# Performance work log

Measured on AMD Instinct MI355X. Metric: run time of the kernel, lower is better.

The kernel has to match this reference:

```python
import jax, jax.numpy as jnp
import numpy as np

N = 8192
FEAT = 128
HID = 128
EMB = 128
NHEADS = 2
RO_HID = 256
G_EMB = 128
ALPHA = 0.2          # LeakyReLU negative slope
NEG_INF = -9e15      # matches -9000000000000000.0 in the torch source


def _xavier(k, shape, gain=1.0):
    fan_in, fan_out = shape[-2], shape[-1]
    s = gain * np.sqrt(2.0 / (fan_in + fan_out))
    return jax.random.normal(k, shape, jnp.float32) * jnp.float32(s)


def setup_inputs() -> dict:
    key = jax.random.key(0)
    ks = jax.random.split(key, 10)
    adj = jax.random.randint(ks[0], (N, N), 0, 2, jnp.int32)          # dense 0/1 adjacency
    x = jax.random.normal(ks[1], (N, FEAT), jnp.float32)
    W_heads = _xavier(ks[2], (NHEADS, FEAT, HID), gain=1.414)
    a_heads = _xavier(ks[3], (NHEADS, 2 * HID, 1), gain=1.414)
    W_out = _xavier(ks[4], (NHEADS * HID, EMB), gain=1.414)
    a_out = _xavier(ks[5], (2 * EMB, 1), gain=1.414)
    ge_w1 = _xavier(ks[6], (FEAT + EMB, RO_HID))
    ge_b1 = jnp.zeros((RO_HID,), jnp.float32)
    ge_w2 = _xavier(ks[7], (RO_HID, G_EMB))
    ge_b2 = jnp.zeros((G_EMB,), jnp.float32)
    return dict(adj=adj, feature_matrix=x, W_heads=W_heads, a_heads=a_heads,
                W_out=W_out, a_out=a_out, ge_w1=ge_w1, ge_b1=ge_b1,
                ge_w2=ge_w2, ge_b2=ge_b2, supply=0)


def _gat_layer(x, mask, W, a, concat):
    # Faithful to GraphAttentionLayer: e_ij = leakyrelu([Wh_i || Wh_j] @ a).
    # The concat-then-matmul decomposes exactly as Wh@a[:F] + (Wh@a[F:])^T,
    # avoiding the O(N^2 * 2F) a_input tensor while computing identical math.
    Wh = x @ W                                   # [N, F]
    F_out = W.shape[1]
    f1 = (Wh @ a[:F_out]).squeeze(-1)            # [N]
    f2 = (Wh @ a[F_out:]).squeeze(-1)            # [N]
    e = jax.nn.leaky_relu(f1[:, None] + f2[None, :], ALPHA)   # [N, N]
    e = jnp.where(mask, e, jnp.float32(NEG_INF))
    att = jax.nn.softmax(e, axis=1)              # dropout is identity in eval mode
    h = att @ Wh                                 # [N, F]
    return jax.nn.elu(h) if concat else h


def reference(adj, feature_matrix, W_heads, a_heads, W_out, a_out,
              ge_w1, ge_b1, ge_w2, ge_b2, supply):
    mask = adj > 0
    # GAT: multi-head layer 1 (concat), then out_att (no concat) + elu
    heads = [_gat_layer(feature_matrix, mask, W_heads[i], a_heads[i], True)
             for i in range(NHEADS)]
    h = jnp.concatenate(heads, axis=1)           # [N, NHEADS*HID]
    node_emb = jax.nn.elu(_gat_layer(h, mask, W_out, a_out, False))  # [N, EMB]
    # GraphEmb readout (mode='mean')
    combined = jnp.concatenate([feature_matrix, node_emb], axis=1)   # [N, FEAT+EMB]
    h1 = jax.nn.relu(combined @ ge_w1 + ge_b1)
    h2 = jax.nn.relu(h1 @ ge_w2 + ge_b2)
    graph_emb = jnp.mean(h2, axis=0)             # [G_EMB]
    return node_emb, graph_emb
```

## Files before the change

### kernel.cpp

```cpp
#include <hip/hip_runtime.h>
#include <hip/hip_bf16.h>

typedef unsigned short u16;
typedef __attribute__((ext_vector_type(4))) float f32x4;
typedef __attribute__((ext_vector_type(8))) short bf16x8;
typedef __attribute__((ext_vector_type(4))) unsigned short u16x4;

#define N 8192
#define LOG2E 1.4426950408889634f

__device__ __forceinline__ float bf2f(u16 u){
  union { float f; unsigned int i; } v; v.i = ((unsigned int)u) << 16; return v.f;
}
__device__ __forceinline__ u16 f2bf(float f){
  union { float f; unsigned int i; } v; v.f = f;
  unsigned int r = v.i + 0x7fffu + ((v.i >> 16) & 1u);
  return (u16)(r >> 16);
}
__device__ __forceinline__ f32x4 mfma16(bf16x8 a, bf16x8 b, f32x4 c){
  return __builtin_amdgcn_mfma_f32_16x16x32_bf16(a, b, c, 0, 0, 0);
}

__global__ __launch_bounds__(256) void k_pack(const int* __restrict__ adj,
                                              unsigned long long* __restrict__ packed){
  const int wid = blockIdx.x * 4 + (threadIdx.x >> 6);
  const int lane = threadIdx.x & 63;
  const size_t base = (size_t)wid * 128;
  #pragma unroll 4
  for (int g = 0; g < 128; ++g){
    const size_t grp = base + g;
    const int v = adj[grp * 64 + lane];
    const unsigned long long m = __ballot(v != 0);
    if (lane == 0){
      const unsigned int lo = (unsigned int)m, hi = (unsigned int)(m >> 32);
      const unsigned int olo = __builtin_amdgcn_perm(hi, lo, 0x05010400u);
      const unsigned int ohi = __builtin_amdgcn_perm(hi, lo, 0x07030602u);
      packed[grp] = ((unsigned long long)ohi << 32) | olo;
    }
  }
}

__global__ __launch_bounds__(256) void k_x2bf(const float* __restrict__ x,
                                              u16* __restrict__ xbf, u16* __restrict__ comb){
  const int idx = blockIdx.x * 256 + threadIdx.x;
  f32x4 v = ((const f32x4*)x)[idx];
  u16x4 h;
  #pragma unroll
  for (int e = 0; e < 4; ++e) h[e] = f2bf(v[e]);
  ((u16x4*)xbf)[idx] = h;
  const int i = idx >> 5, c4 = (idx & 31) * 4;
  *(u16x4*)(comb + (size_t)i * 256 + c4) = h;
}

__global__ void k_transpose(const float* __restrict__ src, u16* __restrict__ dst,
                            int K, int Ncols){
  const size_t boff = (size_t)blockIdx.y * K * Ncols;
  const int idx = blockIdx.x * 256 + threadIdx.x;
  if (idx >= K * Ncols) return;
  const int n = idx / K, k = idx % K;
  dst[boff + idx] = f2bf(src[boff + (size_t)k * Ncols + n]);
}

__global__ __launch_bounds__(256) void k_wa(const float* __restrict__ Wh, const float* __restrict__ ah,
                                            const float* __restrict__ Wo, const float* __restrict__ ao,
                                            float* __restrict__ wa){
  const int z = blockIdx.x, t = threadIdx.x;
  if (z < 2){
    if (t < 128){
      float a1 = 0.f, a2 = 0.f;
      for (int c = 0; c < 128; ++c){
        const float w = Wh[(size_t)z * 16384 + t * 128 + c];
        a1 += w * ah[z * 256 + c];
        a2 += w * ah[z * 256 + 128 + c];
      }
      wa[z * 128 + t] = a1; wa[256 + z * 128 + t] = a2;
    }
  } else {
    if (t < 256){
      float a1 = 0.f, a2 = 0.f;
      for (int c = 0; c < 128; ++c){
        const float w = Wo[(size_t)t * 128 + c];
        a1 += w * ao[c];
        a2 += w * ao[128 + c];
      }
      wa[512 + t] = a1; wa[768 + t] = a2;
    }
  }
}

__global__ __launch_bounds__(256) void k_gemv1(const float* __restrict__ x, const float* __restrict__ wa,
                                               float* __restrict__ f1s, float* __restrict__ f2s){
  const int h = blockIdx.y;
  const float* wa1 = wa + h * 128;
  const float* wa2 = wa + 256 + h * 128;
  const int lane = threadIdx.x & 63, w = threadIdx.x >> 6;
  const int r16 = lane & 15, g4 = lane >> 4;
  const int row = blockIdx.x * 16 + w * 4 + g4;
  const float* xr = x + (size_t)row * 128 + r16 * 8;
  f32x4 x0 = *(const f32x4*)(xr);
  f32x4 x1 = *(const f32x4*)(xr + 4);
  f32x4 wA0 = *(const f32x4*)(wa1 + r16 * 8);
  f32x4 wA1 = *(const f32x4*)(wa1 + r16 * 8 + 4);
  f32x4 wB0 = *(const f32x4*)(wa2 + r16 * 8);
  f32x4 wB1 = *(const f32x4*)(wa2 + r16 * 8 + 4);
  float d1 = 0.f, d2 = 0.f;
  #pragma unroll
  for (int e = 0; e < 4; ++e){
    d1 += x0[e] * wA0[e] + x1[e] * wA1[e];
    d2 += x0[e] * wB0[e] + x1[e] * wB1[e];
  }
  d1 += __shfl_xor(d1, 1); d1 += __shfl_xor(d1, 2); d1 += __shfl_xor(d1, 4); d1 += __shfl_xor(d1, 8);
  d2 += __shfl_xor(d2, 1); d2 += __shfl_xor(d2, 2); d2 += __shfl_xor(d2, 4); d2 += __shfl_xor(d2, 8);
  if (r16 == 0){
    f1s[(size_t)h * N + row] = d1 * LOG2E;
    f2s[(size_t)h * N + row] = d2 * LOG2E;
  }
}

__global__ __launch_bounds__(256) void k_gemv2(const u16* __restrict__ hbf,
                                               const float* __restrict__ wao1, const float* __restrict__ wao2,
                                               float* __restrict__ f1s, float* __restrict__ f2s){
  const int lane = threadIdx.x & 63, w = threadIdx.x >> 6;
  const int r16 = lane & 15, g4 = lane >> 4;
  const int row = blockIdx.x * 16 + w * 4 + g4;
  bf16x8 h0 = *(const bf16x8*)(hbf + (size_t)row * 256 + r16 * 16);
  bf16x8 h1 = *(const bf16x8*)(hbf + (size_t)row * 256 + r16 * 16 + 8);
  float d1 = 0.f, d2 = 0.f;
  #pragma unroll
  for (int e = 0; e < 8; ++e){
    const float v0 = bf2f((u16)h0[e]), v1 = bf2f((u16)h1[e]);
    d1 += v0 * wao1[r16 * 16 + e] + v1 * wao1[r16 * 16 + 8 + e];
    d2 += v0 * wao2[r16 * 16 + e] + v1 * wao2[r16 * 16 + 8 + e];
  }
  d1 += __shfl_xor(d1, 1); d1 += __shfl_xor(d1, 2); d1 += __shfl_xor(d1, 4); d1 += __shfl_xor(d1, 8);
  d2 += __shfl_xor(d2, 1); d2 += __shfl_xor(d2, 2); d2 += __shfl_xor(d2, 4); d2 += __shfl_xor(d2, 8);
  if (r16 == 0){
    f1s[row] = d1 * LOG2E;
    f2s[row] = d2 * LOG2E;
  }
}

__global__ __launch_bounds__(256) void k_fmax(const float* __restrict__ f2s, float* __restrict__ fmax){
  const int h = blockIdx.x;
  const float* f = f2s + (size_t)h * N;
  float m = -3e38f;
  for (int i = threadIdx.x; i < N; i += 256) m = fmaxf(m, f[i]);
  m = fmaxf(m, __shfl_xor(m, 1));  m = fmaxf(m, __shfl_xor(m, 2));
  m = fmaxf(m, __shfl_xor(m, 4));  m = fmaxf(m, __shfl_xor(m, 8));
  m = fmaxf(m, __shfl_xor(m, 16)); m = fmaxf(m, __shfl_xor(m, 32));
  __shared__ float sm[4];
  if ((threadIdx.x & 63) == 0) sm[threadIdx.x >> 6] = m;
  __syncthreads();
  if (threadIdx.x == 0) fmax[h] = fmaxf(fmaxf(sm[0], sm[1]), fmaxf(sm[2], sm[3]));
}

__global__ __launch_bounds__(256) void k_gemm_at(const u16* __restrict__ A_all, const u16* __restrict__ B,
                                                 u16* __restrict__ outT_all, int K){
  const int head = blockIdx.y;
  const u16* A = A_all + (size_t)head * 128 * K;
  u16* outT = outT_all + (size_t)head * 128 * N;
  const int lane = threadIdx.x & 63, w = threadIdx.x >> 6;
  const int r16 = lane & 15, g4 = lane >> 4;
  const size_t ib = (size_t)blockIdx.x * 64 + w * 16;
  f32x4 acc[8];
  #pragma unroll
  for (int cg = 0; cg < 8; ++cg) acc[cg] = (f32x4){0,0,0,0};
  for (int kk = 0; kk < K; kk += 32){
    bf16x8 b = *(const bf16x8*)(B + (ib + r16) * (size_t)K + kk + g4 * 8);
    #pragma unroll
    for (int cg = 0; cg < 8; ++cg){
      bf16x8 a = *(const bf16x8*)(A + (size_t)(cg * 16 + r16) * K + kk + g4 * 8);
      acc[cg] = mfma16(a, b, acc[cg]);
    }
  }
  #pragma unroll
  for (int cg = 0; cg < 8; ++cg)
    #pragma unroll
    for (int q = 0; q < 4; ++q)
      outT[(size_t)(cg * 16 + g4 * 4 + q) * N + ib + r16] = f2bf(acc[cg][q]);
}

template<int S>
__global__ __launch_bounds__(64, 3) void k_attn(
    const unsigned char* __restrict__ pk,
    const u16* __restrict__ whT_all,
    const float* __restrict__ f1_all, const float* __restrict__ f2_all,
    const float* __restrict__ fmax_all,
    u16* __restrict__ part, float* __restrict__ pl)
{
  const int h = blockIdx.z;
  const int s = blockIdx.y;
  const u16* whT = whT_all + (size_t)h * 128 * N;
  const float* f2 = f2_all + (size_t)h * N;
  const float fmax = fmax_all[h];
  const int lane = threadIdx.x;
  const int r16 = lane & 15, g4 = lane >> 4;
  const size_t ibase = (size_t)blockIdx.x * 32;
  const int t0 = (s * 128) / S, t1 = ((s + 1) * 128) / S;

  float c1[2], c2[2];
  f32x4 acc[2][8];
  f32x4 accl[2];
  #pragma unroll
  for (int rg = 0; rg < 2; ++rg){
    const float f1v = f1_all[(size_t)h * N + ibase + rg * 16 + r16];
    const float y = f1v + fmax;
    const float mrow = fmaxf(y, 0.2f * y);
    c1[rg] = f1v - mrow;
    c2[rg] = fmaf(0.2f, f1v, -mrow);
    accl[rg] = (f32x4){0,0,0,0};
    #pragma unroll
    for (int ct = 0; ct < 8; ++ct) acc[rg][ct] = (f32x4){0,0,0,0};
  }
  bf16x8 ones;
  #pragma unroll
  for (int e = 0; e < 8; ++e) ones[e] = (short)0x3F80;

  const unsigned char* pkr0 = pk + (ibase + r16) * 1024 + g4 * 2;
  const unsigned char* pkr1 = pkr0 + 16 * 1024;
  const float* f2p = f2 + g4 * 8;
  unsigned int bc0 = *(const unsigned short*)(pkr0 + t0 * 8);
  unsigned int bc1 = *(const unsigned short*)(pkr1 + t0 * 8);
  f32x4 f2r0 = *(const f32x4*)(f2p + t0 * 64);
  f32x4 f2r1 = *(const f32x4*)(f2p + t0 * 64 + 4);
  f32x4 f2r2 = *(const f32x4*)(f2p + t0 * 64 + 32);
  f32x4 f2r3 = *(const f32x4*)(f2p + t0 * 64 + 36);

  for (int t = t0; t < t1; ++t){
    const u16* bp = whT + (size_t)r16 * N + t * 64 + g4 * 8;
    bf16x8 b0[8];
    #pragma unroll
    for (int ct = 0; ct < 8; ++ct) b0[ct] = *(const bf16x8*)(bp + (size_t)ct * 16 * N);
    unsigned int bn0, bn1; f32x4 f2n0, f2n1, f2n2, f2n3;
    if (t + 1 < t1){
      bn0 = *(const unsigned short*)(pkr0 + (t + 1) * 8);
      bn1 = *(const unsigned short*)(pkr1 + (t + 1) * 8);
      f2n0 = *(const f32x4*)(f2p + (t + 1) * 64);
      f2n1 = *(const f32x4*)(f2p + (t + 1) * 64 + 4);
      f2n2 = *(const f32x4*)(f2p + (t + 1) * 64 + 32);
      f2n3 = *(const f32x4*)(f2p + (t + 1) * 64 + 36);
    } else {
      bn0 = bc0; bn1 = bc1; f2n0 = f2r0; f2n1 = f2r1; f2n2 = f2r2; f2n3 = f2r3;
    }
    bf16x8 pa[2][2];
    #pragma unroll
    for (int k2 = 0; k2 < 2; ++k2){
      const f32x4 fa = k2 ? f2r2 : f2r0;
      const f32x4 fb = k2 ? f2r3 : f2r1;
      const float fsv[8] = {fa[0], fa[1], fa[2], fa[3], fb[0], fb[1], fb[2], fb[3]};
      #pragma unroll
      for (int rg = 0; rg < 2; ++rg){
        const unsigned int bb = ((rg ? bc1 : bc0) >> (k2 * 8)) & 0xFFu;
        union { __hip_bfloat162 h2[4]; bf16x8 v8; } u;
        #pragma unroll
        for (int xp = 0; xp < 4; ++xp){
          const float s0 = fsv[2 * xp], s1 = fsv[2 * xp + 1];
          float p0 = __builtin_amdgcn_exp2f(fmaxf(s0 + c1[rg], fmaf(s0, 0.2f, c2[rg])));
          float p1 = __builtin_amdgcn_exp2f(fmaxf(s1 + c1[rg], fmaf(s1, 0.2f, c2[rg])));
          p0 = ((bb >> (2 * xp)) & 1u) ? p0 : 0.f;
          p1 = ((bb >> (2 * xp + 1)) & 1u) ? p1 : 0.f;
          u.h2[xp] = __float22bfloat162_rn(make_float2(p0, p1));
        }
        pa[rg][k2] = u.v8;
        accl[rg] = mfma16(pa[rg][k2], ones, accl[rg]);
      }
    }
    #pragma unroll
    for (int ct = 0; ct < 8; ++ct){
      acc[0][ct] = mfma16(pa[0][0], b0[ct], acc[0][ct]);
      acc[1][ct] = mfma16(pa[1][0], b0[ct], acc[1][ct]);
    }
    #pragma unroll
    for (int ct = 0; ct < 8; ++ct){
      bf16x8 b1 = *(const bf16x8*)(bp + (size_t)ct * 16 * N + 32);
      acc[0][ct] = mfma16(pa[0][1], b1, acc[0][ct]);
      acc[1][ct] = mfma16(pa[1][1], b1, acc[1][ct]);
    }
    bc0 = bn0; bc1 = bn1; f2r0 = f2n0; f2r1 = f2n1; f2r2 = f2n2; f2r3 = f2n3;
  }

  const int plane = h * S + s;
  u16* pp = part + (size_t)plane * (size_t)N * 128;
  #pragma unroll
  for (int rg = 0; rg < 2; ++rg){
    if (r16 == 0){
      #pragma unroll
      for (int q = 0; q < 4; ++q)
        pl[(size_t)plane * N + ibase + rg * 16 + g4 * 4 + q] = accl[rg][q];
    }
    #pragma unroll
    for (int ct = 0; ct < 8; ++ct)
      #pragma unroll
      for (int q = 0; q < 4; ++q)
        pp[(ibase + rg * 16 + g4 * 4 + q) * 128 + ct * 16 + r16] = f2bf(acc[rg][ct][q]);
  }
}

template<int S, bool L2>
__global__ __launch_bounds__(256) void k_attn_merge(
    const u16* __restrict__ part, const float* __restrict__ pl,
    u16* __restrict__ hbf, float* __restrict__ nodeout, u16* __restrict__ comb)
{
  const int h = blockIdx.y;
  const int idx = blockIdx.x * 256 + threadIdx.x;
  const int i = idx >> 5, c4 = (idx & 31) * 4;
  f32x4 a = (f32x4){0,0,0,0};
  float L = 0.f;
  #pragma unroll
  for (int s = 0; s < S; ++s){
    const size_t plane = h * S + s;
    u16x4 v = *(const u16x4*)(part + plane * (size_t)N * 128 + (size_t)i * 128 + c4);
    a[0] += bf2f(v[0]); a[1] += bf2f(v[1]); a[2] += bf2f(v[2]); a[3] += bf2f(v[3]);
    L += pl[plane * (size_t)N + i];
  }
  const float linv = 1.f / L;
  u16x4 hv;
  #pragma unroll
  for (int e = 0; e < 4; ++e){
    float o = a[e] * linv;
    o = (o > 0.f) ? o : (__expf(o) - 1.f);
    a[e] = o;
    hv[e] = f2bf(o);
  }
  if constexpr (!L2){
    *(u16x4*)(hbf + (size_t)i * 256 + h * 128 + c4) = hv;
  } else {
    *(f32x4*)(nodeout + (size_t)i * 128 + c4) = a;
    *(u16x4*)(comb + (size_t)i * 256 + 128 + c4) = hv;
  }
}

template<bool STORE, bool COLSUM>
__global__ __launch_bounds__(256) void k_gemm_row(
    const u16* __restrict__ A, const u16* __restrict__ BT,
    const float* __restrict__ bias,
    u16* __restrict__ out, float* __restrict__ csum,
    int K, int Ntot)
{
  const int lane = threadIdx.x & 63, w = threadIdx.x >> 6;
  const int r16 = lane & 15, g4 = lane >> 4;
  const size_t rbase = (size_t)blockIdx.x * 64 + w * 16;
  const int cbase = blockIdx.y * 128;
  f32x4 acc[8];
  #pragma unroll
  for (int ct = 0; ct < 8; ++ct) acc[ct] = (f32x4){0,0,0,0};
  for (int kk = 0; kk < K; kk += 32){
    bf16x8 af = *(const bf16x8*)(A + (rbase + r16) * (size_t)K + kk + g4 * 8);
    #pragma unroll
    for (int ct = 0; ct < 8; ++ct){
      bf16x8 bfr = *(const bf16x8*)(BT + (size_t)(cbase + ct * 16 + r16) * K + kk + g4 * 8);
      acc[ct] = mfma16(af, bfr, acc[ct]);
    }
  }
  #pragma unroll
  for (int ct = 0; ct < 8; ++ct){
    const float bv = bias[cbase + ct * 16 + r16];
    float sacc = 0.f;
    #pragma unroll
    for (int q = 0; q < 4; ++q){
      float v = acc[ct][q] + bv;
      v = fmaxf(v, 0.f);
      if constexpr (STORE)
        out[(rbase + g4 * 4 + q) * (size_t)Ntot + cbase + ct * 16 + r16] = f2bf(v);
      sacc += v;
    }
    if constexpr (COLSUM){
      sacc += __shfl_xor(sacc, 16); sacc += __shfl_xor(sacc, 32);
      if (lane < 16) atomicAdd(&csum[cbase + ct * 16 + lane], sacc);
    }
  }
}

__global__ void k_final(const float* __restrict__ csum, float* __restrict__ out){
  out[threadIdx.x] = csum[threadIdx.x] * (1.f / 8192.f);
}

extern "C" void kernel_launch(void* const* d_in, const int* in_sizes, int n_in,
                              void* d_out, int out_size, void* d_ws, size_t ws_size,
                              hipStream_t stream) {
  const int*   adj = (const int*)d_in[0];
  const float* x   = (const float*)d_in[1];
  const float* Wh  = (const float*)d_in[2];
  const float* ah  = (const float*)d_in[3];
  const float* Wo  = (const float*)d_in[4];
  const float* ao  = (const float*)d_in[5];
  const float* g1  = (const float*)d_in[6];
  const float* b1  = (const float*)d_in[7];
  const float* g2  = (const float*)d_in[8];
  const float* b2  = (const float*)d_in[9];
  float* outp = (float*)d_out;
  char* ws = (char*)d_ws;

  constexpr size_t PK   = 0;
  constexpr size_t PART = 8388608;
  constexpr size_t PL   = 33554432;
  constexpr size_t XBF  = 33947648;
  constexpr size_t WHT1 = 36044800;
  constexpr size_t WHT2 = 40239104;
  constexpr size_t HBF  = 42336256;
  constexpr size_t COMB = 46530560;
  constexpr size_t H1RO = 50724864;
  constexpr size_t F1S  = 54919168;
  constexpr size_t F2S  = 54984704;
  constexpr size_t FMAX = 55050240;
  constexpr size_t CSUM = 55050496;
  constexpr size_t WTH  = 55051008;
  constexpr size_t WOT  = 55116544;
  constexpr size_t G1T  = 55182080;
  constexpr size_t G2T  = 55313152;
  constexpr size_t WA   = 55378688;

  hipMemsetAsync(ws + CSUM, 0, 512, stream);

  k_pack<<<2048, 256, 0, stream>>>(adj, (unsigned long long*)(ws + PK));
  k_x2bf<<<1024, 256, 0, stream>>>(x, (u16*)(ws + XBF), (u16*)(ws + COMB));
  k_transpose<<<dim3(64, 2), 256, 0, stream>>>(Wh, (u16*)(ws + WTH), 128, 128);
  k_transpose<<<dim3(128, 1), 256, 0, stream>>>(Wo, (u16*)(ws + WOT), 256, 128);
  k_transpose<<<dim3(256, 1), 256, 0, stream>>>(g1, (u16*)(ws + G1T), 256, 256);
  k_transpose<<<dim3(128, 1), 256, 0, stream>>>(g2, (u16*)(ws + G2T), 256, 128);
  k_wa<<<3, 256, 0, stream>>>(Wh, ah, Wo, ao, (float*)(ws + WA));

  k_gemv1<<<dim3(512, 2), 256, 0, stream>>>(x, (const float*)(ws + WA),
                                            (float*)(ws + F1S), (float*)(ws + F2S));
  k_fmax<<<2, 256, 0, stream>>>((const float*)(ws + F2S), (float*)(ws + FMAX));
  k_gemm_at<<<dim3(128, 2), 256, 0, stream>>>((const u16*)(ws + WTH), (const u16*)(ws + XBF),
                                              (u16*)(ws + WHT1), 128);
  k_attn<6><<<dim3(256, 6, 2), 64, 0, stream>>>(
      (const unsigned char*)(ws + PK), (const u16*)(ws + WHT1),
      (const float*)(ws + F1S), (const float*)(ws + F2S), (const float*)(ws + FMAX),
      (u16*)(ws + PART), (float*)(ws + PL));
  k_attn_merge<6, false><<<dim3(1024, 2), 256, 0, stream>>>(
      (const u16*)(ws + PART), (const float*)(ws + PL),
      (u16*)(ws + HBF), nullptr, nullptr);

  k_gemv2<<<dim3(512, 1), 256, 0, stream>>>((const u16*)(ws + HBF),
      (const float*)(ws + WA) + 512, (const float*)(ws + WA) + 768,
      (float*)(ws + F1S), (float*)(ws + F2S));
  k_fmax<<<1, 256, 0, stream>>>((const float*)(ws + F2S), (float*)(ws + FMAX));
  k_gemm_at<<<dim3(128, 1), 256, 0, stream>>>((const u16*)(ws + WOT), (const u16*)(ws + HBF),
                                              (u16*)(ws + WHT2), 256);
  k_attn<12><<<dim3(256, 12, 1), 64, 0, stream>>>(
      (const unsigned char*)(ws + PK), (const u16*)(ws + WHT2),
      (const float*)(ws + F1S), (const float*)(ws + F2S), (const float*)(ws + FMAX),
      (u16*)(ws + PART), (float*)(ws + PL));
  k_attn_merge<12, true><<<dim3(1024, 1), 256, 0, stream>>>(
      (const u16*)(ws + PART), (const float*)(ws + PL),
      nullptr, outp, (u16*)(ws + COMB));

  k_gemm_row<true, false><<<dim3(128, 2), 256, 0, stream>>>(
      (const u16*)(ws + COMB), (const u16*)(ws + G1T), b1,
      (u16*)(ws + H1RO), nullptr, 256, 256);
  k_gemm_row<false, true><<<dim3(128, 1), 256, 0, stream>>>(
      (const u16*)(ws + H1RO), (const u16*)(ws + G2T), b2,
      nullptr, (float*)(ws + CSUM), 256, 128);
  k_final<<<1, 128, 0, stream>>>((const float*)(ws + CSUM), outp + (size_t)N * 128);
}
```

Baseline: 790.1 us.

## Fuse prep kernels, fold column max into GEMV atomics, reshape attention tiling

Merges the bf16 conversion, weight transposes, wa precompute and zero-initialisation into a single prep kernel, removing several launches and the memset. The separate column-max kernels are dropped: each GEMV wave now does an atomicMax on an order-preserving uint key. The attention kernel moves from 64-thread blocks handling 32 rows each to 256-thread blocks where each wave handles 16 rows, so each wave uses fewer registers but the per-wave reuse of the loaded Wh tiles is halved. Partial outputs are written in an MFMA-fragment tile layout that the merge kernel reads back with matching index arithmetic, giving coalesced stores.

```diff
diff --git a/kernel.cpp b/kernel.cpp
--- a/kernel.cpp
+++ b/kernel.cpp
@@ -19,6 +19,14 @@
 }
 __device__ __forceinline__ f32x4 mfma16(bf16x8 a, bf16x8 b, f32x4 c){
   return __builtin_amdgcn_mfma_f32_16x16x32_bf16(a, b, c, 0, 0, 0);
+}
+__device__ __forceinline__ unsigned int fkey_enc(float f){
+  unsigned int u = __float_as_uint(f);
+  return (u & 0x80000000u) ? ~u : (u | 0x80000000u);
+}
+__device__ __forceinline__ float fkey_dec(unsigned int k){
+  unsigned int u = (k & 0x80000000u) ? (k ^ 0x80000000u) : ~k;
+  return __uint_as_float(u);
 }
 
 __global__ __launch_bounds__(256) void k_pack(const int* __restrict__ adj,
@@ -40,56 +48,74 @@
   }
 }
 
-__global__ __launch_bounds__(256) void k_x2bf(const float* __restrict__ x,
-                                              u16* __restrict__ xbf, u16* __restrict__ comb){
-  const int idx = blockIdx.x * 256 + threadIdx.x;
-  f32x4 v = ((const f32x4*)x)[idx];
-  u16x4 h;
-  #pragma unroll
-  for (int e = 0; e < 4; ++e) h[e] = f2bf(v[e]);
-  ((u16x4*)xbf)[idx] = h;
-  const int i = idx >> 5, c4 = (idx & 31) * 4;
-  *(u16x4*)(comb + (size_t)i * 256 + c4) = h;
-}
-
-__global__ void k_transpose(const float* __restrict__ src, u16* __restrict__ dst,
-                            int K, int Ncols){
-  const size_t boff = (size_t)blockIdx.y * K * Ncols;
-  const int idx = blockIdx.x * 256 + threadIdx.x;
-  if (idx >= K * Ncols) return;
-  const int n = idx / K, k = idx % K;
-  dst[boff + idx] = f2bf(src[boff + (size_t)k * Ncols + n]);
-}
-
-__global__ __launch_bounds__(256) void k_wa(const float* __restrict__ Wh, const float* __restrict__ ah,
-                                            const float* __restrict__ Wo, const float* __restrict__ ao,
-                                            float* __restrict__ wa){
-  const int z = blockIdx.x, t = threadIdx.x;
-  if (z < 2){
-    if (t < 128){
-      float a1 = 0.f, a2 = 0.f;
-      for (int c = 0; c < 128; ++c){
-        const float w = Wh[(size_t)z * 16384 + t * 128 + c];
-        a1 += w * ah[z * 256 + c];
-        a2 += w * ah[z * 256 + 128 + c];
+__global__ __launch_bounds__(256) void k_prep(
+    const float* __restrict__ x, const float* __restrict__ Wh, const float* __restrict__ Wo,
+    const float* __restrict__ g1, const float* __restrict__ g2,
+    const float* __restrict__ ah, const float* __restrict__ ao,
+    u16* __restrict__ xbf, u16* __restrict__ comb,
+    u16* __restrict__ wth, u16* __restrict__ wot,
+    u16* __restrict__ g1t, u16* __restrict__ g2t,
+    float* __restrict__ wa, unsigned int* __restrict__ fkey, float* __restrict__ csum)
+{
+  const int b = blockIdx.x, t = threadIdx.x;
+  if (b < 1024){
+    const int idx = b * 256 + t;
+    f32x4 v = ((const f32x4*)x)[idx];
+    u16x4 h;
+    #pragma unroll
+    for (int e = 0; e < 4; ++e) h[e] = f2bf(v[e]);
+    ((u16x4*)xbf)[idx] = h;
+    const int i = idx >> 5, c4 = (idx & 31) * 4;
+    *(u16x4*)(comb + (size_t)i * 256 + c4) = h;
+  } else if (b < 1152){
+    const int rel = (b - 1024) * 256 + t;
+    const int head = rel >> 14, win = rel & 16383;
+    const int n = win >> 7, k = win & 127;
+    wth[rel] = f2bf(Wh[(head << 14) + k * 128 + n]);
+  } else if (b < 1280){
+    const int rel = (b - 1152) * 256 + t;
+    const int n = rel >> 8, k = rel & 255;
+    wot[rel] = f2bf(Wo[k * 128 + n]);
+  } else if (b < 1536){
+    const int rel = (b - 1280) * 256 + t;
+    const int n = rel >> 8, k = rel & 255;
+    g1t[rel] = f2bf(g1[k * 256 + n]);
+  } else if (b < 1664){
+    const int rel = (b - 1536) * 256 + t;
+    const int n = rel >> 8, k = rel & 255;
+    g2t[rel] = f2bf(g2[k * 128 + n]);
+  } else if (b < 1667){
+    const int z = b - 1664;
+    if (z < 2){
+      if (t < 128){
+        float a1 = 0.f, a2 = 0.f;
+        for (int c = 0; c < 128; ++c){
+          const float w = Wh[(size_t)z * 16384 + t * 128 + c];
+          a1 += w * ah[z * 256 + c];
+          a2 += w * ah[z * 256 + 128 + c];
+        }
+        wa[z * 128 + t] = a1; wa[256 + z * 128 + t] = a2;
       }
-      wa[z * 128 + t] = a1; wa[256 + z * 128 + t] = a2;
+    } else {
+      if (t < 256){
+        float a1 = 0.f, a2 = 0.f;
+        for (int c = 0; c < 128; ++c){
+          const float w = Wo[(size_t)t * 128 + c];
+          a1 += w * ao[c];
+          a2 += w * ao[128 + c];
+        }
+        wa[512 + t] = a1; wa[768 + t] = a2;
+      }
     }
   } else {
-    if (t < 256){
-      float a1 = 0.f, a2 = 0.f;
-      for (int c = 0; c < 128; ++c){
-        const float w = Wo[(size_t)t * 128 + c];
-        a1 += w * ao[c];
-        a2 += w * ao[128 + c];
-      }
-      wa[512 + t] = a1; wa[768 + t] = a2;
-    }
+    if (t < 128) csum[t] = 0.f;
+    if (t < 4) fkey[t] = 0u;
   }
 }
 
 __global__ __launch_bounds__(256) void k_gemv1(const float* __restrict__ x, const float* __restrict__ wa,
-                                               float* __restrict__ f1s, float* __restrict__ f2s){
+                                               float* __restrict__ f1s, float* __restrict__ f2s,
+                                               unsigned int* __restrict__ fkey){
   const int h = blockIdx.y;
   const float* wa1 = wa + h * 128;
   const float* wa2 = wa + 256 + h * 128;
@@ -111,15 +137,20 @@
   }
   d1 += __shfl_xor(d1, 1); d1 += __shfl_xor(d1, 2); d1 += __shfl_xor(d1, 4); d1 += __shfl_xor(d1, 8);
   d2 += __shfl_xor(d2, 1); d2 += __shfl_xor(d2, 2); d2 += __shfl_xor(d2, 4); d2 += __shfl_xor(d2, 8);
+  const float d1s = d1 * LOG2E, d2s = d2 * LOG2E;
   if (r16 == 0){
-    f1s[(size_t)h * N + row] = d1 * LOG2E;
-    f2s[(size_t)h * N + row] = d2 * LOG2E;
-  }
+    f1s[(size_t)h * N + row] = d1s;
+    f2s[(size_t)h * N + row] = d2s;
+  }
+  float m = d2s;
+  m = fmaxf(m, __shfl_xor(m, 16)); m = fmaxf(m, __shfl_xor(m, 32));
+  if (lane == 0) atomicMax(fkey + h, fkey_enc(m));
 }
 
 __global__ __launch_bounds__(256) void k_gemv2(const u16* __restrict__ hbf,
                                                const float* __restrict__ wao1, const float* __restrict__ wao2,
-                                               float* __restrict__ f1s, float* __restrict__ f2s){
+                                               float* __restrict__ f1s, float* __restrict__ f2s,
+                                               unsigned int* __restrict__ fkey){
   const int lane = threadIdx.x & 63, w = threadIdx.x >> 6;
   const int r16 = lane & 15, g4 = lane >> 4;
   const int row = blockIdx.x * 16 + w * 4 + g4;
@@ -134,24 +165,14 @@
   }
   d1 += __shfl_xor(d1, 1); d1 += __shfl_xor(d1, 2); d1 += __shfl_xor(d1, 4); d1 += __shfl_xor(d1, 8);
   d2 += __shfl_xor(d2, 1); d2 += __shfl_xor(d2, 2); d2 += __shfl_xor(d2, 4); d2 += __shfl_xor(d2, 8);
+  const float d1s = d1 * LOG2E, d2s = d2 * LOG2E;
   if (r16 == 0){
-    f1s[row] = d1 * LOG2E;
-    f2s[row] = d2 * LOG2E;
-  }
-}
-
-__global__ __launch_bounds__(256) void k_fmax(const float* __restrict__ f2s, float* __restrict__ fmax){
-  const int h = blockIdx.x;
-  const float* f = f2s + (size_t)h * N;
-  float m = -3e38f;
-  for (int i = threadIdx.x; i < N; i += 256) m = fmaxf(m, f[i]);
-  m = fmaxf(m, __shfl_xor(m, 1));  m = fmaxf(m, __shfl_xor(m, 2));
-  m = fmaxf(m, __shfl_xor(m, 4));  m = fmaxf(m, __shfl_xor(m, 8));
+    f1s[row] = d1s;
+    f2s[row] = d2s;
+  }
+  float m = d2s;
   m = fmaxf(m, __shfl_xor(m, 16)); m = fmaxf(m, __shfl_xor(m, 32));
-  __shared__ float sm[4];
-  if ((threadIdx.x & 63) == 0) sm[threadIdx.x >> 6] = m;
-  __syncthreads();
-  if (threadIdx.x == 0) fmax[h] = fmaxf(fmaxf(sm[0], sm[1]), fmaxf(sm[2], sm[3]));
+  if (lane == 0) atomicMax(fkey, fkey_enc(m));
 }
 
 __global__ __launch_bounds__(256) void k_gemm_at(const u16* __restrict__ A_all, const u16* __restrict__ B,
@@ -181,46 +202,41 @@
 }
 
 template<int S>
-__global__ __launch_bounds__(64, 3) void k_attn(
+__global__ __launch_bounds__(256, 4) void k_attn(
     const unsigned char* __restrict__ pk,
     const u16* __restrict__ whT_all,
     const float* __restrict__ f1_all, const float* __restrict__ f2_all,
-    const float* __restrict__ fmax_all,
+    const unsigned int* __restrict__ fkey,
     u16* __restrict__ part, float* __restrict__ pl)
 {
   const int h = blockIdx.z;
   const int s = blockIdx.y;
   const u16* whT = whT_all + (size_t)h * 128 * N;
   const float* f2 = f2_all + (size_t)h * N;
-  const float fmax = fmax_all[h];
-  const int lane = threadIdx.x;
+  const float fmax = fkey_dec(fkey[h]);
+  const int w = threadIdx.x >> 6;
+  const int lane = threadIdx.x & 63;
   const int r16 = lane & 15, g4 = lane >> 4;
-  const size_t ibase = (size_t)blockIdx.x * 32;
+  const int tile_row = blockIdx.x * 4 + w;
+  const size_t ibase = (size_t)tile_row * 16;
   const int t0 = (s * 128) / S, t1 = ((s + 1) * 128) / S;
 
-  float c1[2], c2[2];
-  f32x4 acc[2][8];
-  f32x4 accl[2];
-  #pragma unroll
-  for (int rg = 0; rg < 2; ++rg){
-    const float f1v = f1_all[(size_t)h * N + ibase + rg * 16 + r16];
-    const float y = f1v + fmax;
-    const float mrow = fmaxf(y, 0.2f * y);
-    c1[rg] = f1v - mrow;
-    c2[rg] = fmaf(0.2f, f1v, -mrow);
-    accl[rg] = (f32x4){0,0,0,0};
-    #pragma unroll
-    for (int ct = 0; ct < 8; ++ct) acc[rg][ct] = (f32x4){0,0,0,0};
-  }
+  const float f1v = f1_all[(size_t)h * N + ibase + r16];
+  const float y = f1v + fmax;
+  const float mrow = fmaxf(y, 0.2f * y);
+  const float c1 = f1v - mrow;
+  const float c2 = fmaf(0.2f, f1v, -mrow);
+  f32x4 acc[8];
+  f32x4 accl = (f32x4){0,0,0,0};
+  #pragma unroll
+  for (int ct = 0; ct < 8; ++ct) acc[ct] = (f32x4){0,0,0,0};
   bf16x8 ones;
   #pragma unroll
   for (int e = 0; e < 8; ++e) ones[e] = (short)0x3F80;
 
-  const unsigned char* pkr0 = pk + (ibase + r16) * 1024 + g4 * 2;
-  const unsigned char* pkr1 = pkr0 + 16 * 1024;
+  const unsigned char* pkr = pk + (ibase + r16) * 1024 + g4 * 2;
   const float* f2p = f2 + g4 * 8;
-  unsigned int bc0 = *(const unsigned short*)(pkr0 + t0 * 8);
-  unsigned int bc1 = *(const unsigned short*)(pkr1 + t0 * 8);
+  unsigned int bc = *(const unsigned short*)(pkr + t0 * 8);
   f32x4 f2r0 = *(const f32x4*)(f2p + t0 * 64);
   f32x4 f2r1 = *(const f32x4*)(f2p + t0 * 64 + 4);
   f32x4 f2r2 = *(const f32x4*)(f2p + t0 * 64 + 32);
@@ -231,68 +247,58 @@
     bf16x8 b0[8];
     #pragma unroll
     for (int ct = 0; ct < 8; ++ct) b0[ct] = *(const bf16x8*)(bp + (size_t)ct * 16 * N);
-    unsigned int bn0, bn1; f32x4 f2n0, f2n1, f2n2, f2n3;
+    unsigned int bn; f32x4 f2n0, f2n1, f2n2, f2n3;
     if (t + 1 < t1){
-      bn0 = *(const unsigned short*)(pkr0 + (t + 1) * 8);
-      bn1 = *(const unsigned short*)(pkr1 + (t + 1) * 8);
+      bn = *(const unsigned short*)(pkr + (t + 1) * 8);
       f2n0 = *(const f32x4*)(f2p + (t + 1) * 64);
       f2n1 = *(const f32x4*)(f2p + (t + 1) * 64 + 4);
       f2n2 = *(const f32x4*)(f2p + (t + 1) * 64 + 32);
       f2n3 = *(const f32x4*)(f2p + (t + 1) * 64 + 36);
     } else {
-      bn0 = bc0; bn1 = bc1; f2n0 = f2r0; f2n1 = f2r1; f2n2 = f2r2; f2n3 = f2r3;
-    }
-    bf16x8 pa[2][2];
+      bn = bc; f2n0 = f2r0; f2n1 = f2r1; f2n2 = f2r2; f2n3 = f2r3;
+    }
+    bf16x8 pa[2];
     #pragma unroll
     for (int k2 = 0; k2 < 2; ++k2){
       const f32x4 fa = k2 ? f2r2 : f2r0;
       const f32x4 fb = k2 ? f2r3 : f2r1;
       const float fsv[8] = {fa[0], fa[1], fa[2], fa[3], fb[0], fb[1], fb[2], fb[3]};
+      const unsigned int bb = (bc >> (k2 * 8)) & 0xFFu;
+      union { __hip_bfloat162 h2[4]; bf16x8 v8; } u;
       #pragma unroll
-      for (int rg = 0; rg < 2; ++rg){
-        const unsigned int bb = ((rg ? bc1 : bc0) >> (k2 * 8)) & 0xFFu;
-        union { __hip_bfloat162 h2[4]; bf16x8 v8; } u;
-        #pragma unroll
-        for (int xp = 0; xp < 4; ++xp){
-          const float s0 = fsv[2 * xp], s1 = fsv[2 * xp + 1];
-          float p0 = __builtin_amdgcn_exp2f(fmaxf(s0 + c1[rg], fmaf(s0, 0.2f, c2[rg])));
-          float p1 = __builtin_amdgcn_exp2f(fmaxf(s1 + c1[rg], fmaf(s1, 0.2f, c2[rg])));
-          p0 = ((bb >> (2 * xp)) & 1u) ? p0 : 0.f;
-          p1 = ((bb >> (2 * xp + 1)) & 1u) ? p1 : 0.f;
-          u.h2[xp] = __float22bfloat162_rn(make_float2(p0, p1));
-        }
-        pa[rg][k2] = u.v8;
-        accl[rg] = mfma16(pa[rg][k2], ones, accl[rg]);
+      for (int xp = 0; xp < 4; ++xp){
+        const float s0 = fsv[2 * xp], s1 = fsv[2 * xp + 1];
+        float p0 = __builtin_amdgcn_exp2f(fmaxf(s0 + c1, fmaf(s0, 0.2f, c2)));
+        float p1 = __builtin_amdgcn_exp2f(fmaxf(s1 + c1, fmaf(s1, 0.2f, c2)));
+        p0 = ((bb >> (2 * xp)) & 1u) ? p0 : 0.f;
+        p1 = ((bb >> (2 * xp + 1)) & 1u) ? p1 : 0.f;
+        u.h2[xp] = __float22bfloat162_rn(make_float2(p0, p1));
       }
-    }
-    #pragma unroll
-    for (int ct = 0; ct < 8; ++ct){
-      acc[0][ct] = mfma16(pa[0][0], b0[ct], acc[0][ct]);
-      acc[1][ct] = mfma16(pa[1][0], b0[ct], acc[1][ct]);
-    }
+      pa[k2] = u.v8;
+      accl = mfma16(pa[k2], ones, accl);
+    }
+    #pragma unroll
+    for (int ct = 0; ct < 8; ++ct)
+      acc[ct] = mfma16(pa[0], b0[ct], acc[ct]);
     #pragma unroll
     for (int ct = 0; ct < 8; ++ct){
       bf16x8 b1 = *(const bf16x8*)(bp + (size_t)ct * 16 * N + 32);
-      acc[0][ct] = mfma16(pa[0][1], b1, acc[0][ct]);
-      acc[1][ct] = mfma16(pa[1][1], b1, acc[1][ct]);
-    }
-    bc0 = bn0; bc1 = bn1; f2r0 = f2n0; f2r1 = f2n1; f2r2 = f2n2; f2r3 = f2n3;
+      acc[ct] = mfma16(pa[1], b1, acc[ct]);
+    }
+    bc = bn; f2r0 = f2n0; f2r1 = f2n1; f2r2 = f2n2; f2r3 = f2n3;
   }
 
   const int plane = h * S + s;
-  u16* pp = part + (size_t)plane * (size_t)N * 128;
-  #pragma unroll
-  for (int rg = 0; rg < 2; ++rg){
-    if (r16 == 0){
-      #pragma unroll
-      for (int q = 0; q < 4; ++q)
-        pl[(size_t)plane * N + ibase + rg * 16 + g4 * 4 + q] = accl[rg][q];
-    }
-    #pragma unroll
-    for (int ct = 0; ct < 8; ++ct)
-      #pragma unroll
-      for (int q = 0; q < 4; ++q)
-        pp[(ibase + rg * 16 + g4 * 4 + q) * 128 + ct * 16 + r16] = f2bf(acc[rg][ct][q]);
+  u16* pp = part + ((size_t)plane * 512 + tile_row) * 2048;
+  #pragma unroll
+  for (int ct = 0; ct < 8; ++ct)
+    #pragma unroll
+    for (int q = 0; q < 4; ++q)
+      pp[(ct * 4 + q) * 64 + lane] = f2bf(acc[ct][q]);
+  if (r16 == 0){
+    #pragma unroll
+    for (int q = 0; q < 4; ++q)
+      pl[(size_t)plane * N + ibase + g4 * 4 + q] = accl[q];
   }
 }
 
@@ -304,12 +310,14 @@
   const int h = blockIdx.y;
   const int idx = blockIdx.x * 256 + threadIdx.x;
   const int i = idx >> 5, c4 = (idx & 31) * 4;
+  const int tile = i >> 4, r = i & 15;
+  const size_t off = (size_t)tile * 2048 + (size_t)(((c4 >> 4) * 4 + (r & 3)) * 64 + ((r >> 2) & 3) * 16 + (c4 & 15));
   f32x4 a = (f32x4){0,0,0,0};
   float L = 0.f;
   #pragma unroll
   for (int s = 0; s < S; ++s){
     const size_t plane = h * S + s;
-    u16x4 v = *(const u16x4*)(part + plane * (size_t)N * 128 + (size_t)i * 128 + c4);
+    u16x4 v = *(const u16x4*)(part + plane * (size_t)(N * 128) + off);
     a[0] += bf2f(v[0]); a[1] += bf2f(v[1]); a[2] += bf2f(v[2]); a[3] += bf2f(v[3]);
     L += pl[plane * (size_t)N + i];
   }
@@ -402,32 +410,27 @@
   constexpr size_t H1RO = 50724864;
   constexpr size_t F1S  = 54919168;
   constexpr size_t F2S  = 54984704;
-  constexpr size_t FMAX = 55050240;
-  constexpr size_t CSUM = 55050496;
+  constexpr size_t CSUM = 55050240;
   constexpr size_t WTH  = 55051008;
   constexpr size_t WOT  = 55116544;
   constexpr size_t G1T  = 55182080;
   constexpr size_t G2T  = 55313152;
   constexpr size_t WA   = 55378688;
-
-  hipMemsetAsync(ws + CSUM, 0, 512, stream);
+  constexpr size_t FKEY = 55382784;
 
   k_pack<<<2048, 256, 0, stream>>>(adj, (unsigned long long*)(ws + PK));
-  k_x2bf<<<1024, 256, 0, stream>>>(x, (u16*)(ws + XBF), (u16*)(ws + COMB));
-  k_transpose<<<dim3(64, 2), 256, 0, stream>>>(Wh, (u16*)(ws + WTH), 128, 128);
-  k_transpose<<<dim3(128, 1), 256, 0, stream>>>(Wo, (u16*)(ws + WOT), 256, 128);
-  k_transpose<<<dim3(256, 1), 256, 0, stream>>>(g1, (u16*)(ws + G1T), 256, 256);
-  k_transpose<<<dim3(128, 1), 256, 0, stream>>>(g2, (u16*)(ws + G2T), 256, 128);
-  k_wa<<<3, 256, 0, stream>>>(Wh, ah, Wo, ao, (float*)(ws + WA));
+  k_prep<<<1668, 256, 0, stream>>>(x, Wh, Wo, g1, g2, ah, ao,
+      (u16*)(ws + XBF), (u16*)(ws + COMB), (u16*)(ws + WTH), (u16*)(ws + WOT),
+      (u16*)(ws + G1T), (u16*)(ws + G2T),
+      (float*)(ws + WA), (unsigned int*)(ws + FKEY), (float*)(ws + CSUM));
 
   k_gemv1<<<dim3(512, 2), 256, 0, stream>>>(x, (const float*)(ws + WA),
-                                            (float*)(ws + F1S), (float*)(ws + F2S));
-  k_fmax<<<2, 256, 0, stream>>>((const float*)(ws + F2S), (float*)(ws + FMAX));
+      (float*)(ws + F1S), (float*)(ws + F2S), (unsigned int*)(ws + FKEY));
   k_gemm_at<<<dim3(128, 2), 256, 0, stream>>>((const u16*)(ws + WTH), (const u16*)(ws + XBF),
                                               (u16*)(ws + WHT1), 128);
-  k_attn<6><<<dim3(256, 6, 2), 64, 0, stream>>>(
+  k_attn<6><<<dim3(128, 6, 2), 256, 0, stream>>>(
       (const unsigned char*)(ws + PK), (const u16*)(ws + WHT1),
-      (const float*)(ws + F1S), (const float*)(ws + F2S), (const float*)(ws + FMAX),
+      (const float*)(ws + F1S), (const float*)(ws + F2S), (const unsigned int*)(ws + FKEY),
       (u16*)(ws + PART), (float*)(ws + PL));
   k_attn_merge<6, false><<<dim3(1024, 2), 256, 0, stream>>>(
       (const u16*)(ws + PART), (const float*)(ws + PL),
@@ -435,13 +438,12 @@
 
   k_gemv2<<<dim3(512, 1), 256, 0, stream>>>((const u16*)(ws + HBF),
       (const float*)(ws + WA) + 512, (const float*)(ws + WA) + 768,
-      (float*)(ws + F1S), (float*)(ws + F2S));
-  k_fmax<<<1, 256, 0, stream>>>((const float*)(ws + F2S), (float*)(ws + FMAX));
+      (float*)(ws + F1S), (float*)(ws + F2S), (unsigned int*)(ws + FKEY) + 2);
   k_gemm_at<<<dim3(128, 1), 256, 0, stream>>>((const u16*)(ws + WOT), (const u16*)(ws + HBF),
                                               (u16*)(ws + WHT2), 256);
-  k_attn<12><<<dim3(256, 12, 1), 64, 0, stream>>>(
+  k_attn<12><<<dim3(128, 12, 1), 256, 0, stream>>>(
       (const unsigned char*)(ws + PK), (const u16*)(ws + WHT2),
-      (const float*)(ws + F1S), (const float*)(ws + F2S), (const float*)(ws + FMAX),
+      (const float*)(ws + F1S), (const float*)(ws + F2S), (const unsigned int*)(ws + FKEY) + 2,
       (u16*)(ws + PART), (float*)(ws + PL));
   k_attn_merge<12, true><<<dim3(1024, 1), 256, 0, stream>>>(
       (const u16*)(ws + PART), (const float*)(ws + PL),
```

Result: slower. 1.014 ms (+28.4%).
